# Performance work log

Hardware: AMD Instinct MI355X
Metric: run time of the kernel (lower is better)

Reference implementation:

```python
import jax, jax.numpy as jnp
import numpy as np

B, L = 64, 512
D_IN, D_POS = 256, 64
KS, VS, H = 64, 64, 8
OUT = 256
EPS = 1e-5
NEG = -1e30


def setup_inputs() -> dict:
    key = jax.random.key(0)
    ks = jax.random.split(key, 12)
    D = D_IN + D_POS
    s = 0.02
    return {
        "emb": jax.random.normal(ks[0], (B, L, D_IN), jnp.float32),
        "boxes": jax.random.normal(ks[1], (B, L, D_POS), jnp.float32),
        "lengths": jax.random.randint(ks[2], (B,), 1, L + 1, jnp.int32),
        "Wq": jax.random.normal(ks[3], (D, H * KS), jnp.float32) * s,
        "Wk": jax.random.normal(ks[4], (D, H * KS), jnp.float32) * s,
        "Wv": jax.random.normal(ks[5], (D, H * VS), jnp.float32) * s,
        "W1": jax.random.normal(ks[6], (H * VS, OUT), jnp.float32) * s,
        "b1": jnp.zeros((OUT,), jnp.float32),
        "W2": jax.random.normal(ks[7], (OUT, OUT), jnp.float32) * s,
        "b2": jnp.zeros((OUT,), jnp.float32),
        "g1": jnp.ones((OUT,), jnp.float32),
        "be1": jnp.zeros((OUT,), jnp.float32),
        "g2": jnp.ones((OUT,), jnp.float32),
        "be2": jnp.zeros((OUT,), jnp.float32),
    }


def masked_bn(x, m, cnt, gamma, beta):
    # BatchNorm1d (training stats) over valid tokens only; x: [B,L,C], m: [B,L,1]
    mean = jnp.sum(x * m, axis=(0, 1)) / cnt
    var = jnp.sum(((x - mean) ** 2) * m, axis=(0, 1)) / cnt
    return gamma * (x - mean) * jax.lax.rsqrt(var + EPS) + beta


def reference(emb, boxes, lengths, Wq, Wk, Wv, W1, b1, W2, b2, g1, be1, g2, be2):
    X = jnp.concatenate([emb, boxes], axis=-1)  # [B,L,D]
    valid = (jnp.arange(L)[None, :] < lengths[:, None])  # [B,L] bool
    m = valid[..., None].astype(X.dtype)  # [B,L,1]
    cnt = jnp.sum(m)

    D = X.shape[-1]
    Q = jnp.einsum('bld,dhk->bhlk', X, Wq.reshape(D, H, KS))
    K = jnp.einsum('bld,dhk->bhlk', X, Wk.reshape(D, H, KS))
    V = jnp.einsum('bld,dhv->bhlv', X, Wv.reshape(D, H, VS))

    scores = jnp.einsum('bhqk,bhmk->bhqm', Q, K) / jnp.sqrt(jnp.float32(KS))
    scores = jnp.where(valid[:, None, None, :], scores, NEG)  # mask keys
    A = jax.nn.softmax(scores, axis=-1)  # [B,H,L,L]
    Z = jnp.einsum('bhqm,bhmv->bhqv', A, V)  # [B,H,L,V]
    Z = jnp.transpose(Z, (0, 2, 1, 3)).reshape(B, L, H * VS)

    # agregate: Linear -> BN -> ReLU -> (dropout=identity, eval) -> Linear -> BN + skip -> ReLU
    Z1 = Z @ W1 + b1
    Z1 = jax.nn.relu(masked_bn(Z1, m, cnt, g1, be1)) * m
    Z2 = Z1 @ W2 + b2
    out = jax.nn.relu(masked_bn(Z2, m, cnt, g2, be2) + emb) * m
    return out  # padded [B,L,OUT]; invalid positions zeroed
```

## Files before the change

kernel.cpp:

```cpp
#include <hip/hip_runtime.h>
#include <hip/hip_bf16.h>
#include <cstdio>

#define B_    64
#define L_    512
#define DIN   256
#define DPOS  64
#define DD    320
#define HH    8
#define ROWS  (B_*L_)
#define NQKV  1536

typedef __attribute__((ext_vector_type(4))) float floatx4;
typedef __attribute__((ext_vector_type(8))) __bf16 bf16x8;
typedef __attribute__((ext_vector_type(4))) __bf16 bf16x4;

static __device__ __forceinline__ floatx4 mfma_bf16(bf16x8 a, bf16x8 b, floatx4 c) {
  return __builtin_amdgcn_mfma_f32_16x16x32_bf16(a, b, c, 0, 0, 0);
}

#define GLOAD_LDS(gp, lp) \
  __builtin_amdgcn_global_load_lds((const __attribute__((address_space(1))) void*)(gp), \
                                   (__attribute__((address_space(3))) void*)(lp), 16, 0, 0)

__global__ __launch_bounds__(256)
void prep_x(const float* __restrict__ emb, const float* __restrict__ boxes,
            __hip_bfloat16* __restrict__ X) {
  int bb = blockIdx.x;
  if (bb < ROWS/4) {
    int idx = bb * 256 + threadIdx.x;
    int row = idx >> 6, c4 = (idx & 63) * 4;
    const float4 v = *(const float4*)(emb + (size_t)idx * 4);
    bf16x4 o; o[0] = (__bf16)v.x; o[1] = (__bf16)v.y; o[2] = (__bf16)v.z; o[3] = (__bf16)v.w;
    *(bf16x4*)((__bf16*)X + (size_t)row * DD + c4) = o;
  } else {
    int idx = (bb - ROWS/4) * 256 + threadIdx.x;
    int row = idx >> 4, c4 = (idx & 15) * 4;
    const float4 v = *(const float4*)(boxes + (size_t)idx * 4);
    bf16x4 o; o[0] = (__bf16)v.x; o[1] = (__bf16)v.y; o[2] = (__bf16)v.z; o[3] = (__bf16)v.w;
    *(bf16x4*)((__bf16*)X + (size_t)row * DD + DIN + c4) = o;
  }
}

__global__ __launch_bounds__(256)
void prep_w(const float* __restrict__ Wq, const float* __restrict__ Wk,
            const float* __restrict__ Wv, const float* __restrict__ W1,
            const float* __restrict__ W2,
            __hip_bfloat16* __restrict__ WqkvT, __hip_bfloat16* __restrict__ W1T,
            __hip_bfloat16* __restrict__ W2T) {
  __shared__ float tile[64][65];
  int blk = blockIdx.x, t = threadIdx.x;
  const float* src; __hip_bfloat16* dst; int n0, k0, ldsrc, lddst;
  if (blk < 120) {
    int m = blk / 40, rel = blk % 40;
    src = (m == 0) ? Wq : (m == 1) ? Wk : Wv;
    dst = WqkvT + (size_t)m * 512 * DD;
    n0 = (rel / 5) * 64; k0 = (rel % 5) * 64; ldsrc = 512; lddst = DD;
  } else if (blk < 152) {
    int rel = blk - 120;
    src = W1; dst = W1T; n0 = (rel >> 3) * 64; k0 = (rel & 7) * 64; ldsrc = 256; lddst = 512;
  } else {
    int rel = blk - 152;
    src = W2; dst = W2T; n0 = (rel >> 2) * 64; k0 = (rel & 3) * 64; ldsrc = 256; lddst = 256;
  }
#pragma unroll
  for (int i = 0; i < 16; ++i) {
    int e = i * 256 + t, kr = e >> 6, nc = e & 63;
    tile[kr][nc] = src[(size_t)(k0 + kr) * ldsrc + n0 + nc];
  }
  __syncthreads();
#pragma unroll
  for (int i = 0; i < 4; ++i) {
    int ww = i * 256 + t, nr = ww >> 4, kc = (ww & 15) * 4;
    bf16x4 o;
    o[0] = (__bf16)tile[kc][nr];   o[1] = (__bf16)tile[kc+1][nr];
    o[2] = (__bf16)tile[kc+2][nr]; o[3] = (__bf16)tile[kc+3][nr];
    *(bf16x4*)(dst + (size_t)(n0 + nr) * lddst + k0 + kc) = o;
  }
}

template<int EPI>
__global__ __launch_bounds__(256)
void gemm_bt(const __hip_bfloat16* __restrict__ A, const __hip_bfloat16* __restrict__ BT,
             int nbx, int N, int K, int lda,
             float* __restrict__ outF, const float* __restrict__ bias,
             __hip_bfloat16* __restrict__ outQK, __hip_bfloat16* __restrict__ outVT,
             const int* __restrict__ lengths, float* __restrict__ pS,
             float* __restrict__ pS2) {
  __shared__ __align__(16) __bf16 sm[32768];
  int hw = blockIdx.x;
  int lidx = (hw & 7) * ((int)gridDim.x >> 3) + (hw >> 3);
  int bx = lidx % nbx, by = lidx / nbx;
  int t = threadIdx.x;
  int m0 = by * 128, n0 = bx * 128;
  int lenb = lengths[m0 >> 9];
  if ((m0 & 511) >= lenb) {
    if (EPI == 1 && t < 128) {
      pS [by*256 + bx*128 + t] = 0.f;
      pS2[by*256 + bx*128 + t] = 0.f;
    }
    return;
  }
  int wave = t >> 6, lane = t & 63, lr = lane & 15, lg = lane >> 4;
  int wr = wave >> 1, wc = wave & 1;
  floatx4 acc[4][4];
#pragma unroll
  for (int i = 0; i < 4; ++i)
#pragma unroll
    for (int j = 0; j < 4; ++j)
#pragma unroll
      for (int q = 0; q < 4; ++q) acc[i][j][q] = 0.f;

  int srow = t >> 3;
  int scb = (t & 7) ^ (srow & 7);
  const __bf16* gA = (const __bf16*)A + (size_t)(m0 + srow) * lda + scb * 8;
  const __bf16* gB = (const __bf16*)BT + (size_t)(n0 + srow) * K + scb * 8;

  auto stage = [&](int k0, int buf) {
    __bf16* Ad = sm + buf * 8192;
    __bf16* Bd = sm + 16384 + buf * 8192;
#pragma unroll
    for (int r = 0; r < 4; ++r) {
      GLOAD_LDS(gA + (size_t)(r*32) * lda + k0, Ad + (r*256 + t) * 8);
      GLOAD_LDS(gB + (size_t)(r*32) * K   + k0, Bd + (r*256 + t) * 8);
    }
  };

  int aoff[4][2], boff[4][2];
#pragma unroll
  for (int i = 0; i < 4; ++i) {
#pragma unroll
    for (int ks = 0; ks < 2; ++ks) {
      int ra = wr*64 + i*16 + lr;
      int rb = wc*64 + i*16 + lr;
      aoff[i][ks] = ra*64 + (((ks*4 + lg) ^ (ra & 7)) * 8);
      boff[i][ks] = rb*64 + (((ks*4 + lg) ^ (rb & 7)) * 8);
    }
  }

  int NK = K >> 6;
  stage(0, 0);
  __syncthreads();
  for (int kt = 0; kt < NK; ++kt) {
    int cur = kt & 1;
    if (kt + 1 < NK) stage((kt + 1) << 6, cur ^ 1);
    const __bf16* As = sm + cur * 8192;
    const __bf16* Bs = sm + 16384 + cur * 8192;
#pragma unroll
    for (int ks = 0; ks < 2; ++ks) {
      bf16x8 af[4], bfr[4];
#pragma unroll
      for (int i = 0; i < 4; ++i) af[i]  = *(const bf16x8*)(As + aoff[i][ks]);
#pragma unroll
      for (int j = 0; j < 4; ++j) bfr[j] = *(const bf16x8*)(Bs + boff[j][ks]);
      __builtin_amdgcn_s_setprio(1);
#pragma unroll
      for (int i = 0; i < 4; ++i)
#pragma unroll
        for (int j = 0; j < 4; ++j)
          acc[i][j] = mfma_bf16(af[i], bfr[j], acc[i][j]);
      __builtin_amdgcn_s_setprio(0);
    }
    __syncthreads();
  }

  if (EPI == 1) {
    int lbase = m0 & 511;
    float s1[4] = {0.f,0.f,0.f,0.f}, s2[4] = {0.f,0.f,0.f,0.f};
#pragma unroll
    for (int i = 0; i < 4; ++i)
#pragma unroll
      for (int j = 0; j < 4; ++j)
#pragma unroll
        for (int q = 0; q < 4; ++q) {
          int rrow = wr*64 + i*16 + lg*4 + q;
          int col = n0 + wc*64 + j*16 + lr;
          float v = acc[i][j][q] + bias[col];
          outF[(size_t)(m0 + rrow) * N + col] = v;
          if (lbase + rrow < lenb) { s1[j] += v; s2[j] += v*v; }
        }
#pragma unroll
    for (int j = 0; j < 4; ++j) {
      s1[j] += __shfl_xor(s1[j], 16); s1[j] += __shfl_xor(s1[j], 32);
      s2[j] += __shfl_xor(s2[j], 16); s2[j] += __shfl_xor(s2[j], 32);
    }
    float* fb = (float*)sm;
    if (lg == 0) {
#pragma unroll
      for (int j = 0; j < 4; ++j) {
        int cloc = wc*64 + j*16 + lr;
        fb[wr*128 + cloc] = s1[j];
        fb[256 + wr*128 + cloc] = s2[j];
      }
    }
    __syncthreads();
    if (t < 128) {
      pS [by*256 + bx*128 + t] = fb[t] + fb[128 + t];
      pS2[by*256 + bx*128 + t] = fb[256 + t] + fb[384 + t];
    }
  } else if (n0 < 1024) {
#pragma unroll
    for (int i = 0; i < 4; ++i)
#pragma unroll
      for (int j = 0; j < 4; ++j)
#pragma unroll
        for (int q = 0; q < 4; ++q) {
          int row = m0 + wr*64 + i*16 + lg*4 + q;
          int col = n0 + wc*64 + j*16 + lr;
          outQK[(size_t)row * 1024 + col] = __float2bfloat16(acc[i][j][q]);
        }
  } else {
    __bf16* Ct = sm;
#pragma unroll
    for (int i = 0; i < 4; ++i)
#pragma unroll
      for (int j = 0; j < 4; ++j) {
        int col = wc*64 + j*16 + lr;
        int row0 = wr*64 + i*16 + lg*4;
        bf16x4 pv;
#pragma unroll
        for (int q = 0; q < 4; ++q) pv[q] = (__bf16)acc[i][j][q];
        *(bf16x4*)(Ct + col*136 + row0) = pv;
      }
    __syncthreads();
    int b = m0 >> 9, l0 = m0 & 511, gcol0 = n0 - 1024;
#pragma unroll
    for (int it = 0; it < 8; ++it) {
      int g = it * 256 + t;
      int vv = g >> 4, rc = g & 15;
      bf16x8 val = *(const bf16x8*)(Ct + vv*136 + rc*8);
      int gc = gcol0 + vv, h = gc >> 6, vg = gc & 63;
      *(bf16x8*)((__bf16*)outVT + ((size_t)((b*HH + h)*64 + vg))*512 + l0 + rc*8) = val;
    }
  }
}

__global__ __launch_bounds__(512)
void attn(__hip_bfloat16* QK, const __hip_bfloat16* __restrict__ VT,
          const int* __restrict__ lengths) {
  int hw = blockIdx.x;
  int h = hw & 7, qt = (hw >> 3) & 3, b = hw >> 5;
  int len = lengths[b];
  if (qt * 128 >= len) return;
  __shared__ __align__(16) __hip_bfloat16 Ks[3][2048];
  __shared__ __align__(16) __hip_bfloat16 Vs[3][2048];
  __shared__ __align__(16) __hip_bfloat16 P[8][16][40];
  int t = threadIdx.x, wave = t >> 6, lane = t & 63, lr = lane & 15, lg = lane >> 4;
  int q0 = qt * 128 + wave * 16;
  const __hip_bfloat16* Qb = QK + (size_t)b*512*1024 + h*64;
  const __hip_bfloat16* Kb = QK + (size_t)b*512*1024 + 512 + h*64;
  const __hip_bfloat16* Vb = VT + (size_t)(b*HH + h)*64*512;

  bf16x8 qf0 = *(const bf16x8*)(Qb + (size_t)(q0 + lr)*1024 + lg*8);
  bf16x8 qf1 = *(const bf16x8*)(Qb + (size_t)(q0 + lr)*1024 + 32 + lg*8);
#pragma unroll
  for (int i = 0; i < 8; ++i) {
    qf0[i] = (__bf16)((float)qf0[i] * 0.18033688f);
    qf1[i] = (__bf16)((float)qf1[i] * 0.18033688f);
  }
  bf16x8 onesf;
#pragma unroll
  for (int i = 0; i < 8; ++i) onesf[i] = (__bf16)1.0f;

  int koff0[2], koff1[2];
#pragma unroll
  for (int kb = 0; kb < 2; ++kb) {
    int row = kb*16 + lr, sw = row & 7;
    koff0[kb] = row*64 + ((lg ^ sw) * 8);
    koff1[kb] = row*64 + (((lg + 4) ^ sw) * 8);
  }
  int voff[4];
#pragma unroll
  for (int vb = 0; vb < 4; ++vb) {
    int row = vb*16 + lr;
    voff[vb] = row*32 + ((lg ^ ((row >> 1) & 3)) * 8);
  }
  int ku = t & 255;
  int krow = ku >> 3, kcb = (ku & 7) ^ (krow & 7);
  const __hip_bfloat16* kgp = Kb + (size_t)krow*1024 + kcb*8;
  int vrow = ku >> 2, vcb = (ku & 3) ^ ((vrow >> 1) & 3);
  const __hip_bfloat16* vgp = Vb + (size_t)vrow*512 + vcb*8;

  int nt = (len + 31) >> 5;

  auto stage = [&](int kt, int buf) {
    if (t < 256) GLOAD_LDS(kgp + (size_t)kt*32768, &Ks[buf][ku*8]);
    else         GLOAD_LDS(vgp + kt*32,           &Vs[buf][ku*8]);
  };

  floatx4 O[4];
  floatx4 Ol = {0.f, 0.f, 0.f, 0.f};
#pragma unroll
  for (int vb = 0; vb < 4; ++vb)
#pragma unroll
    for (int i = 0; i < 4; ++i) O[vb][i] = 0.f;

  stage(0, 0);
  if (nt > 1) {
    stage(1, 1);
    asm volatile("s_waitcnt vmcnt(1)" ::: "memory");
  } else {
    asm volatile("s_waitcnt vmcnt(0)" ::: "memory");
  }
  __builtin_amdgcn_sched_barrier(0);
  __builtin_amdgcn_s_barrier();
  __builtin_amdgcn_sched_barrier(0);

  for (int kt = 0; kt < nt; ++kt) {
    int cur = kt % 3;
    if (kt + 2 < nt) stage(kt + 2, (kt + 2) % 3);
    int kb0 = kt * 32;
    const __hip_bfloat16* Kc = Ks[cur];
    const __hip_bfloat16* Vc = Vs[cur];

    floatx4 S[2];
    __builtin_amdgcn_s_setprio(1);
#pragma unroll
    for (int kb = 0; kb < 2; ++kb) {
      bf16x8 kf0 = *(const bf16x8*)(Kc + koff0[kb]);
      bf16x8 kf1 = *(const bf16x8*)(Kc + koff1[kb]);
      floatx4 s = {0.f, 0.f, 0.f, 0.f};
      s = mfma_bf16(kf0, qf0, s);
      s = mfma_bf16(kf1, qf1, s);
      S[kb] = s;
    }
    __builtin_amdgcn_s_setprio(0);
#pragma unroll
    for (int kb = 0; kb < 2; ++kb)
#pragma unroll
      for (int i = 0; i < 4; ++i) S[kb][i] = __builtin_amdgcn_exp2f(S[kb][i]);
    if (kb0 + 32 > len) {
#pragma unroll
      for (int kb = 0; kb < 2; ++kb)
#pragma unroll
        for (int i = 0; i < 4; ++i)
          if (kb0 + kb*16 + lg*4 + i >= len) S[kb][i] = 0.f;
    }
#pragma unroll
    for (int kb = 0; kb < 2; ++kb) {
      bf16x4 pv;
#pragma unroll
      for (int i = 0; i < 4; ++i) pv[i] = (__bf16)S[kb][i];
      *(bf16x4*)(&P[wave][lr][kb*16 + lg*4]) = pv;
    }
    bf16x8 pf = *(const bf16x8*)(&P[wave][lr][lg*8]);
    __builtin_amdgcn_s_setprio(1);
#pragma unroll
    for (int vb = 0; vb < 4; ++vb) {
      bf16x8 vf = *(const bf16x8*)(Vc + voff[vb]);
      O[vb] = mfma_bf16(pf, vf, O[vb]);
    }
    Ol = mfma_bf16(pf, onesf, Ol);
    __builtin_amdgcn_s_setprio(0);

    if (kt + 1 < nt) {
      if (kt + 2 < nt) asm volatile("s_waitcnt vmcnt(1)" ::: "memory");
      else             asm volatile("s_waitcnt vmcnt(0)" ::: "memory");
      __builtin_amdgcn_sched_barrier(0);
      __builtin_amdgcn_s_barrier();
      __builtin_amdgcn_sched_barrier(0);
    }
  }

#pragma unroll
  for (int vb = 0; vb < 4; ++vb)
#pragma unroll
    for (int i = 0; i < 4; ++i) {
      int q = q0 + lg*4 + i;
      float z = O[vb][i] / Ol[i];
      QK[(size_t)(b*512 + q)*1024 + h*64 + vb*16 + lr] = __float2bfloat16(z);
    }
}

__global__ __launch_bounds__(1024)
void stats_fin(const float* __restrict__ pS, const float* __restrict__ pS2,
               const int* __restrict__ lengths, const float* __restrict__ g,
               const float* __restrict__ be, float* __restrict__ aff) {
  __shared__ float red[2048];
  int t = threadIdx.x, col = t & 255, part = t >> 8;
  float s = 0.f, s2 = 0.f;
  for (int i = part*64; i < part*64 + 64; ++i) {
    s += pS[i*256 + col]; s2 += pS2[i*256 + col];
  }
  red[part*256 + col] = s;
  red[1024 + part*256 + col] = s2;
  __syncthreads();
  if (t < 256) {
    float cnt = 0.f;
    for (int i = 0; i < 64; ++i) cnt += (float)lengths[i];
    float fs = red[t] + red[256 + t] + red[512 + t] + red[768 + t];
    float fs2 = red[1024 + t] + red[1280 + t] + red[1536 + t] + red[1792 + t];
    float mean = fs / cnt;
    float var = fs2 / cnt - mean * mean;
    float a = g[t] * rsqrtf(var + 1e-5f);
    aff[t] = a;
    aff[256 + t] = be[t] - mean * a;
  }
}

__global__ __launch_bounds__(256)
void apply1(const float* __restrict__ Zr, const int* __restrict__ lengths,
            const float* __restrict__ aff, __hip_bfloat16* __restrict__ Zn) {
  int idx = blockIdx.x * 256 + threadIdx.x;
  int row = idx >> 6, c4 = (idx & 63) * 4;
  int b = row >> 9, l = row & 511;
  int lenb = lengths[b];
  if (l >= ((lenb + 127) & ~127)) return;
  bool ok = l < lenb;
  float4 v = *(const float4*)(Zr + (size_t)row*256 + c4);
  float4 a = *(const float4*)(aff + c4);
  float4 c = *(const float4*)(aff + 256 + c4);
  bf16x4 o;
  o[0] = (__bf16)(ok ? fmaxf(a.x*v.x + c.x, 0.f) : 0.f);
  o[1] = (__bf16)(ok ? fmaxf(a.y*v.y + c.y, 0.f) : 0.f);
  o[2] = (__bf16)(ok ? fmaxf(a.z*v.z + c.z, 0.f) : 0.f);
  o[3] = (__bf16)(ok ? fmaxf(a.w*v.w + c.w, 0.f) : 0.f);
  *(bf16x4*)((__bf16*)Zn + (size_t)row*256 + c4) = o;
}

__global__ __launch_bounds__(256)
void apply2(const float* __restrict__ Zr, const float* __restrict__ emb,
            const int* __restrict__ lengths, const float* __restrict__ aff,
            float* __restrict__ out) {
  int idx = blockIdx.x * 256 + threadIdx.x;
  int row = idx >> 6, c4 = (idx & 63) * 4;
  int b = row >> 9, l = row & 511;
  size_t base = (size_t)row*256 + c4;
  if (l >= lengths[b]) {
    float4 z = {0.f, 0.f, 0.f, 0.f};
    *(float4*)(out + base) = z;
    return;
  }
  float4 v = *(const float4*)(Zr + base);
  float4 e = *(const float4*)(emb + base);
  float4 a = *(const float4*)(aff + c4);
  float4 c = *(const float4*)(aff + 256 + c4);
  float4 o;
  o.x = fmaxf(a.x*v.x + c.x + e.x, 0.f);
  o.y = fmaxf(a.y*v.y + c.y + e.y, 0.f);
  o.z = fmaxf(a.z*v.z + c.z + e.z, 0.f);
  o.w = fmaxf(a.w*v.w + c.w + e.w, 0.f);
  *(float4*)(out + base) = o;
}

extern "C" void kernel_launch(void* const* d_in, const int* in_sizes, int n_in,
                              void* d_out, int out_size, void* d_ws, size_t ws_size,
                              hipStream_t stream) {
  const float* emb   = (const float*)d_in[0];
  const float* boxes = (const float*)d_in[1];
  const int*   dlen  = (const int*)d_in[2];
  const float* Wq    = (const float*)d_in[3];
  const float* Wk    = (const float*)d_in[4];
  const float* Wv    = (const float*)d_in[5];
  const float* W1    = (const float*)d_in[6];
  const float* b1    = (const float*)d_in[7];
  const float* W2    = (const float*)d_in[8];
  const float* b2    = (const float*)d_in[9];
  const float* g1    = (const float*)d_in[10];
  const float* be1   = (const float*)d_in[11];
  const float* g2    = (const float*)d_in[12];
  const float* be2   = (const float*)d_in[13];
  float* out = (float*)d_out;

  const size_t oWqkvT = 0;
  const size_t oW1T   = 983040;
  const size_t oW2T   = 1245184;
  const size_t oAff1  = 1376256;
  const size_t oAff2  = 1378304;
  const size_t oPS    = 1380352;
  const size_t oPS2   = 1642496;
  const size_t oXbf   = 1904640;
  const size_t oQK    = 22876160;
  const size_t oVT    = 89985024;
  const size_t NEED   = 123539456;
  if (ws_size < NEED) { fprintf(stderr, "ws too small: %zu < %zu\n", ws_size, NEED); return; }

  char* w = (char*)d_ws;
  __hip_bfloat16* WqkvT = (__hip_bfloat16*)(w + oWqkvT);
  __hip_bfloat16* W1T   = (__hip_bfloat16*)(w + oW1T);
  __hip_bfloat16* W2T   = (__hip_bfloat16*)(w + oW2T);
  float* aff1 = (float*)(w + oAff1);
  float* aff2 = (float*)(w + oAff2);
  float* pS   = (float*)(w + oPS);
  float* pS2  = (float*)(w + oPS2);
  __hip_bfloat16* Xbf = (__hip_bfloat16*)(w + oXbf);
  __hip_bfloat16* Z1n = (__hip_bfloat16*)(w + oXbf);
  __hip_bfloat16* QK  = (__hip_bfloat16*)(w + oQK);
  float* Z2raw = (float*)(w + oQK);
  __hip_bfloat16* VT  = (__hip_bfloat16*)(w + oVT);
  float* Z1raw = (float*)(w + oVT);

  prep_x<<<ROWS/4 + ROWS/16, 256, 0, stream>>>(emb, boxes, Xbf);
  prep_w<<<168, 256, 0, stream>>>(Wq, Wk, Wv, W1, W2, WqkvT, W1T, W2T);
  gemm_bt<0><<<12*256, 256, 0, stream>>>(
      Xbf, WqkvT, 12, NQKV, DD, DD, nullptr, nullptr, QK, VT,
      dlen, nullptr, nullptr);
  attn<<<2048, 512, 0, stream>>>(QK, VT, dlen);
  gemm_bt<1><<<2*256, 256, 0, stream>>>(
      QK, W1T, 2, 256, 512, 1024, Z1raw, b1, nullptr, nullptr,
      dlen, pS, pS2);
  stats_fin<<<1, 1024, 0, stream>>>(pS, pS2, dlen, g1, be1, aff1);
  apply1<<<ROWS/4, 256, 0, stream>>>(Z1raw, dlen, aff1, Z1n);
  gemm_bt<1><<<2*256, 256, 0, stream>>>(
      Z1n, W2T, 2, 256, 256, 256, Z2raw, b2, nullptr, nullptr,
      dlen, pS, pS2);
  stats_fin<<<1, 1024, 0, stream>>>(pS, pS2, dlen, g2, be2, aff2);
  apply2<<<ROWS/4, 256, 0, stream>>>(Z2raw, emb, dlen, aff2, out);
}
```

Before: 166.1 us.

## Schedule blocks by length-sorted batch order and store GEMM outputs in bf16

Adds a small kernel that ranks batches by descending length and uses this order to map blocks in the QKV GEMM, attention and aggregation GEMMs, so long sequences are scheduled first and load balance improves. The aggregation GEMM epilogues now write pre-BN activations as bf16 rather than fp32, halving that intermediate traffic in the GEMMs and the apply kernels. This adds one tiny launch and loses some precision in the stored pre-BN values, though the statistics are still accumulated in fp32.

```diff
diff --git a/kernel.cpp b/kernel.cpp
--- a/kernel.cpp
+++ b/kernel.cpp
@@ -22,6 +22,18 @@
 #define GLOAD_LDS(gp, lp) \
   __builtin_amdgcn_global_load_lds((const __attribute__((address_space(1))) void*)(gp), \
                                    (__attribute__((address_space(3))) void*)(lp), 16, 0, 0)
+
+__global__ __launch_bounds__(64)
+void sort_lens(const int* __restrict__ len, int* __restrict__ order) {
+  int b = threadIdx.x;
+  int lb = len[b];
+  int rank = 0;
+  for (int j = 0; j < 64; ++j) {
+    int lj = len[j];
+    if (lj > lb || (lj == lb && j < b)) ++rank;
+  }
+  order[rank] = b;
+}
 
 __global__ __launch_bounds__(256)
 void prep_x(const float* __restrict__ emb, const float* __restrict__ boxes,
@@ -83,17 +95,20 @@
 __global__ __launch_bounds__(256)
 void gemm_bt(const __hip_bfloat16* __restrict__ A, const __hip_bfloat16* __restrict__ BT,
              int nbx, int N, int K, int lda,
-             float* __restrict__ outF, const float* __restrict__ bias,
+             const float* __restrict__ bias,
              __hip_bfloat16* __restrict__ outQK, __hip_bfloat16* __restrict__ outVT,
-             const int* __restrict__ lengths, float* __restrict__ pS,
-             float* __restrict__ pS2) {
+             const int* __restrict__ lengths, const int* __restrict__ order,
+             float* __restrict__ pS, float* __restrict__ pS2) {
   __shared__ __align__(16) __bf16 sm[32768];
   int hw = blockIdx.x;
   int lidx = (hw & 7) * ((int)gridDim.x >> 3) + (hw >> 3);
   int bx = lidx % nbx, by = lidx / nbx;
   int t = threadIdx.x;
-  int m0 = by * 128, n0 = bx * 128;
-  int lenb = lengths[m0 >> 9];
+  int brank = ((by & 31) >> 2) * 8 + (by >> 5);
+  int bb = order[brank];
+  int m0 = bb * 512 + (by & 3) * 128;
+  int n0 = bx * 128;
+  int lenb = lengths[bb];
   if ((m0 & 511) >= lenb) {
     if (EPI == 1 && t < 128) {
       pS [by*256 + bx*128 + t] = 0.f;
@@ -176,7 +191,7 @@
           int rrow = wr*64 + i*16 + lg*4 + q;
           int col = n0 + wc*64 + j*16 + lr;
           float v = acc[i][j][q] + bias[col];
-          outF[(size_t)(m0 + rrow) * N + col] = v;
+          outQK[(size_t)(m0 + rrow) * N + col] = __float2bfloat16(v);
           if (lbase + rrow < lenb) { s1[j] += v; s2[j] += v*v; }
         }
 #pragma unroll
@@ -237,9 +252,11 @@
 
 __global__ __launch_bounds__(512)
 void attn(__hip_bfloat16* QK, const __hip_bfloat16* __restrict__ VT,
-          const int* __restrict__ lengths) {
+          const int* __restrict__ lengths, const int* __restrict__ order) {
   int hw = blockIdx.x;
-  int h = hw & 7, qt = (hw >> 3) & 3, b = hw >> 5;
+  int h = hw & 7, r = hw >> 3;
+  int rank = r >> 2, qt = r & 3;
+  int b = order[rank];
   int len = lengths[b];
   if (qt * 128 >= len) return;
   __shared__ __align__(16) __hip_bfloat16 Ks[3][2048];
@@ -399,7 +416,7 @@
 }
 
 __global__ __launch_bounds__(256)
-void apply1(const float* __restrict__ Zr, const int* __restrict__ lengths,
+void apply1(const __hip_bfloat16* __restrict__ Zr, const int* __restrict__ lengths,
             const float* __restrict__ aff, __hip_bfloat16* __restrict__ Zn) {
   int idx = blockIdx.x * 256 + threadIdx.x;
   int row = idx >> 6, c4 = (idx & 63) * 4;
@@ -407,19 +424,19 @@
   int lenb = lengths[b];
   if (l >= ((lenb + 127) & ~127)) return;
   bool ok = l < lenb;
-  float4 v = *(const float4*)(Zr + (size_t)row*256 + c4);
+  bf16x4 z = *(const bf16x4*)((const __bf16*)Zr + (size_t)row*256 + c4);
   float4 a = *(const float4*)(aff + c4);
   float4 c = *(const float4*)(aff + 256 + c4);
   bf16x4 o;
-  o[0] = (__bf16)(ok ? fmaxf(a.x*v.x + c.x, 0.f) : 0.f);
-  o[1] = (__bf16)(ok ? fmaxf(a.y*v.y + c.y, 0.f) : 0.f);
-  o[2] = (__bf16)(ok ? fmaxf(a.z*v.z + c.z, 0.f) : 0.f);
-  o[3] = (__bf16)(ok ? fmaxf(a.w*v.w + c.w, 0.f) : 0.f);
+  o[0] = (__bf16)(ok ? fmaxf(a.x*(float)z[0] + c.x, 0.f) : 0.f);
+  o[1] = (__bf16)(ok ? fmaxf(a.y*(float)z[1] + c.y, 0.f) : 0.f);
+  o[2] = (__bf16)(ok ? fmaxf(a.z*(float)z[2] + c.z, 0.f) : 0.f);
+  o[3] = (__bf16)(ok ? fmaxf(a.w*(float)z[3] + c.w, 0.f) : 0.f);
   *(bf16x4*)((__bf16*)Zn + (size_t)row*256 + c4) = o;
 }
 
 __global__ __launch_bounds__(256)
-void apply2(const float* __restrict__ Zr, const float* __restrict__ emb,
+void apply2(const __hip_bfloat16* __restrict__ Zr, const float* __restrict__ emb,
             const int* __restrict__ lengths, const float* __restrict__ aff,
             float* __restrict__ out) {
   int idx = blockIdx.x * 256 + threadIdx.x;
@@ -431,15 +448,15 @@
     *(float4*)(out + base) = z;
     return;
   }
-  float4 v = *(const float4*)(Zr + base);
+  bf16x4 zv = *(const bf16x4*)((const __bf16*)Zr + base);
   float4 e = *(const float4*)(emb + base);
   float4 a = *(const float4*)(aff + c4);
   float4 c = *(const float4*)(aff + 256 + c4);
   float4 o;
-  o.x = fmaxf(a.x*v.x + c.x + e.x, 0.f);
-  o.y = fmaxf(a.y*v.y + c.y + e.y, 0.f);
-  o.z = fmaxf(a.z*v.z + c.z + e.z, 0.f);
-  o.w = fmaxf(a.w*v.w + c.w + e.w, 0.f);
+  o.x = fmaxf(a.x*(float)zv[0] + c.x + e.x, 0.f);
+  o.y = fmaxf(a.y*(float)zv[1] + c.y + e.y, 0.f);
+  o.z = fmaxf(a.z*(float)zv[2] + c.z + e.z, 0.f);
+  o.w = fmaxf(a.w*(float)zv[3] + c.w + e.w, 0.f);
   *(float4*)(out + base) = o;
 }
 
@@ -472,7 +489,8 @@
   const size_t oXbf   = 1904640;
   const size_t oQK    = 22876160;
   const size_t oVT    = 89985024;
-  const size_t NEED   = 123539456;
+  const size_t oOrd   = 123539456;
+  const size_t NEED   = 123539712;
   if (ws_size < NEED) { fprintf(stderr, "ws too small: %zu < %zu\n", ws_size, NEED); return; }
 
   char* w = (char*)d_ws;
@@ -486,24 +504,26 @@
   __hip_bfloat16* Xbf = (__hip_bfloat16*)(w + oXbf);
   __hip_bfloat16* Z1n = (__hip_bfloat16*)(w + oXbf);
   __hip_bfloat16* QK  = (__hip_bfloat16*)(w + oQK);
-  float* Z2raw = (float*)(w + oQK);
+  __hip_bfloat16* Z2b = (__hip_bfloat16*)(w + oQK);
   __hip_bfloat16* VT  = (__hip_bfloat16*)(w + oVT);
-  float* Z1raw = (float*)(w + oVT);
-
+  __hip_bfloat16* Z1b = (__hip_bfloat16*)(w + oVT);
+  int* order = (int*)(w + oOrd);
+
+  sort_lens<<<1, 64, 0, stream>>>(dlen, order);
   prep_x<<<ROWS/4 + ROWS/16, 256, 0, stream>>>(emb, boxes, Xbf);
   prep_w<<<168, 256, 0, stream>>>(Wq, Wk, Wv, W1, W2, WqkvT, W1T, W2T);
   gemm_bt<0><<<12*256, 256, 0, stream>>>(
-      Xbf, WqkvT, 12, NQKV, DD, DD, nullptr, nullptr, QK, VT,
-      dlen, nullptr, nullptr);
-  attn<<<2048, 512, 0, stream>>>(QK, VT, dlen);
+      Xbf, WqkvT, 12, NQKV, DD, DD, nullptr, QK, VT,
+      dlen, order, nullptr, nullptr);
+  attn<<<2048, 512, 0, stream>>>(QK, VT, dlen, order);
   gemm_bt<1><<<2*256, 256, 0, stream>>>(
-      QK, W1T, 2, 256, 512, 1024, Z1raw, b1, nullptr, nullptr,
-      dlen, pS, pS2);
+      QK, W1T, 2, 256, 512, 1024, b1, Z1b, nullptr,
+      dlen, order, pS, pS2);
   stats_fin<<<1, 1024, 0, stream>>>(pS, pS2, dlen, g1, be1, aff1);
-  apply1<<<ROWS/4, 256, 0, stream>>>(Z1raw, dlen, aff1, Z1n);
+  apply1<<<ROWS/4, 256, 0, stream>>>(Z1b, dlen, aff1, Z1n);
   gemm_bt<1><<<2*256, 256, 0, stream>>>(
-      Z1n, W2T, 2, 256, 256, 256, Z2raw, b2, nullptr, nullptr,
-      dlen, pS, pS2);
+      Z1n, W2T, 2, 256, 256, 256, b2, Z2b, nullptr,
+      dlen, order, pS, pS2);
   stats_fin<<<1, 1024, 0, stream>>>(pS, pS2, dlen, g2, be2, aff2);
-  apply2<<<ROWS/4, 256, 0, stream>>>(Z2raw, emb, dlen, aff2, out);
-}
+  apply2<<<ROWS/4, 256, 0, stream>>>(Z2b, emb, dlen, aff2, out);
+}
```

New measurement: 163.6 us. About the same (-1.5%).
